# Optimization experiments

Hardware: AMD Instinct MI355X
Metric: run time of the kernel (lower is better)

## Reference

```python
import jax, jax.numpy as jnp
import numpy as np

N, D, E, H, K = 8192, 1024, 8, 256, 2


def setup_inputs() -> dict:
    key = jax.random.key(0)
    ks = jax.random.split(key, 9)
    s = 0.02
    return {
        "x": jax.random.normal(ks[0], (N, D), dtype=jnp.float32),
        "Wg": jax.random.normal(ks[1], (D, E), dtype=jnp.float32) * s,
        "bg": jnp.zeros((E,), dtype=jnp.float32),
        "W1": jax.random.normal(ks[2], (E, D, H), dtype=jnp.float32) * s,
        "b1": jnp.zeros((E, H), dtype=jnp.float32),
        "W2": jax.random.normal(ks[3], (E, H, H), dtype=jnp.float32) * s,
        "b2": jnp.zeros((E, H), dtype=jnp.float32),
        "W3": jax.random.normal(ks[4], (E, H, D), dtype=jnp.float32) * s,
        "b3": jnp.zeros((E, D), dtype=jnp.float32),
    }


def reference(x, Wg, bg, W1, b1, W2, b2, W3, b3):
    # Gating: softmax over experts, then keep only top-k gate values per token.
    gates = jax.nn.softmax(x @ Wg + bg, axis=-1)              # [N, E]
    top_v, top_i = jax.lax.top_k(gates, K)                    # [N, K]
    rows = jnp.arange(gates.shape[0])[:, None]                # [N, 1]
    top_k_gates = jnp.zeros_like(gates).at[rows, top_i].set(top_v)  # [N, E]

    # Dense all-expert MLP (matches original: every expert runs on every token).
    h = jax.nn.relu(jnp.einsum('nd,edh->neh', x, W1) + b1)    # [N, E, H]
    h = jax.nn.relu(jnp.einsum('neh,ehg->neg', h, W2) + b2)   # [N, E, H]  (dropout is eval no-op)
    eo = jax.nn.relu(jnp.einsum('neh,ehd->ned', h, W3) + b3)  # [N, E, D]

    # Combine with masked gates: einsum('...nde,...ne->...nd') with eo in 'ned' layout.
    output = jnp.einsum('ned,ne->nd', eo, top_k_gates)        # [N, D]
    return output
```

## Files before the change

kernel.cpp:

```cpp
#include <hip/hip_runtime.h>
#include <math.h>

#define NTOK 8192
#define DDIM 1024
#define NEXP 8
#define HDIM 256
#define TOPK 2
#define PADM 128
#define CAPS (NTOK * TOPK + NEXP * PADM)
#define NT128 (CAPS / 128)

typedef __attribute__((ext_vector_type(8))) __bf16 bf16x8;
typedef __attribute__((ext_vector_type(4))) float f32x4;

#define GLDS16(g, s)                                                      \
    __builtin_amdgcn_global_load_lds(                                     \
        (const __attribute__((address_space(1))) void*)(g),               \
        (__attribute__((address_space(3))) void*)(s), 16, 0, 0)

static constexpr size_t OFF_TOFF = 128;
static constexpr size_t OFF_ZBUF = 4096;
static constexpr size_t OFF_T2E  = 8192;
static constexpr size_t OFF_T2G  = OFF_T2E + (size_t)NTOK * TOPK * 4;
static constexpr size_t OFF_SLOT = OFF_T2G + (size_t)NTOK * TOPK * 4;
static constexpr size_t OFF_TOK  = OFF_SLOT + (size_t)NTOK * TOPK * 4;
static constexpr size_t OFF_GAT  = OFF_TOK + (size_t)CAPS * 4;
static constexpr size_t OFF_XB   = (OFF_GAT + (size_t)CAPS * 4 + 255) & ~(size_t)255;
static constexpr size_t OFF_W1T  = OFF_XB  + (size_t)NTOK * DDIM * 2;
static constexpr size_t OFF_W2T  = OFF_W1T + (size_t)NEXP * DDIM * HDIM * 2;
static constexpr size_t OFF_W3T  = OFF_W2T + (size_t)NEXP * HDIM * HDIM * 2;
static constexpr size_t OFF_H1   = OFF_W3T + (size_t)NEXP * HDIM * DDIM * 2;
static constexpr size_t OFF_H2   = OFF_H1  + (size_t)CAPS * HDIM * 2;
static constexpr size_t OFF_H3   = OFF_H2  + (size_t)CAPS * HDIM * 2;

static __device__ __forceinline__ unsigned short f2b(float f) {
    __bf16 h = (__bf16)f;
    return __builtin_bit_cast(unsigned short, h);
}
static __device__ __forceinline__ float b2f(unsigned short u) {
    return __builtin_bit_cast(float, ((unsigned)u) << 16);
}

__global__ __launch_bounds__(256) void gate_conv(
    const float* __restrict__ x, const float* __restrict__ Wg,
    const float* __restrict__ bg, unsigned short* __restrict__ xb,
    int* __restrict__ top2e, float* __restrict__ top2g)
{
    const int n = blockIdx.x * 4 + (threadIdx.x >> 6);
    const int lane = threadIdx.x & 63;
    const float* xr = x + (size_t)n * DDIM;
    unsigned short* xbr = xb + (size_t)n * DDIM;

    float acc[NEXP];
#pragma unroll
    for (int e = 0; e < NEXP; ++e) acc[e] = 0.f;

#pragma unroll
    for (int it = 0; it < 4; ++it) {
        const int d = it * 256 + lane * 4;
        const float4 xv = *(const float4*)(xr + d);
        ushort4 u;
        u.x = f2b(xv.x); u.y = f2b(xv.y); u.z = f2b(xv.z); u.w = f2b(xv.w);
        *(ushort4*)(xbr + d) = u;
        const float xa[4] = {xv.x, xv.y, xv.z, xv.w};
#pragma unroll
        for (int q = 0; q < 4; ++q) {
            const float* wr = Wg + (size_t)(d + q) * NEXP;
            const float4 w0 = *(const float4*)wr;
            const float4 w1 = *(const float4*)(wr + 4);
            acc[0] = fmaf(xa[q], w0.x, acc[0]); acc[1] = fmaf(xa[q], w0.y, acc[1]);
            acc[2] = fmaf(xa[q], w0.z, acc[2]); acc[3] = fmaf(xa[q], w0.w, acc[3]);
            acc[4] = fmaf(xa[q], w1.x, acc[4]); acc[5] = fmaf(xa[q], w1.y, acc[5]);
            acc[6] = fmaf(xa[q], w1.z, acc[6]); acc[7] = fmaf(xa[q], w1.w, acc[7]);
        }
    }
#pragma unroll
    for (int off = 32; off > 0; off >>= 1)
#pragma unroll
        for (int e = 0; e < NEXP; ++e) acc[e] += __shfl_down(acc[e], off, 64);

    if (lane == 0) {
        float v[NEXP], mx = -1e30f;
#pragma unroll
        for (int e = 0; e < NEXP; ++e) { v[e] = acc[e] + bg[e]; mx = fmaxf(mx, v[e]); }
        float p[NEXP], s = 0.f;
#pragma unroll
        for (int e = 0; e < NEXP; ++e) { p[e] = expf(v[e] - mx); s += p[e]; }
        const float inv = 1.f / s;
#pragma unroll
        for (int e = 0; e < NEXP; ++e) p[e] *= inv;
        int i0 = 0;
#pragma unroll
        for (int e = 1; e < NEXP; ++e) if (p[e] > p[i0]) i0 = e;
        int i1 = (i0 == 0) ? 1 : 0;
#pragma unroll
        for (int e = 0; e < NEXP; ++e) if (e != i0 && p[e] > p[i1]) i1 = e;
        top2e[n * 2 + 0] = i0;  top2e[n * 2 + 1] = i1;
        top2g[n * 2 + 0] = p[i0]; top2g[n * 2 + 1] = p[i1];
    }
}

__global__ __launch_bounds__(256) void transpose_all(
    const float* __restrict__ W1, const float* __restrict__ W2,
    const float* __restrict__ W3, __bf16* __restrict__ w1t,
    __bf16* __restrict__ w2t, __bf16* __restrict__ w3t)
{
    __shared__ float t[32][33];
    const int e = blockIdx.y;
    int bt = blockIdx.x;
    const float* Wi; __bf16* Wo; int R, C, xt, yt;
    if (bt < 256)      { Wi = W1; Wo = w1t; R = DDIM; C = HDIM; xt = bt & 7;  yt = bt >> 3; }
    else if (bt < 320) { bt -= 256; Wi = W2; Wo = w2t; R = HDIM; C = HDIM; xt = bt & 7;  yt = bt >> 3; }
    else               { bt -= 320; Wi = W3; Wo = w3t; R = HDIM; C = DDIM; xt = bt & 31; yt = bt >> 5; }
    const int r0 = yt * 32, c0 = xt * 32;
    const int tx = threadIdx.x & 31, ty = threadIdx.x >> 5;
    const float* Wie = Wi + (size_t)e * R * C;
    __bf16* Woe = Wo + (size_t)e * C * R;
#pragma unroll
    for (int j = 0; j < 4; ++j)
        t[ty + j * 8][tx] = Wie[(size_t)(r0 + ty + j * 8) * C + c0 + tx];
    __syncthreads();
#pragma unroll
    for (int j = 0; j < 4; ++j)
        Woe[(size_t)(c0 + ty + j * 8) * R + r0 + tx] = (__bf16)t[tx][ty + j * 8];
}

__global__ __launch_bounds__(1024) void route(
    const int* __restrict__ top2e, const float* __restrict__ top2g,
    int* __restrict__ toff, int* __restrict__ tok, float* __restrict__ gat,
    int* __restrict__ slotof, float* __restrict__ zbuf)
{
    const int tid = threadIdx.x;
    const int wv = tid >> 6, ln = tid & 63;
    __shared__ int   waveTot[16][NEXP];
    __shared__ int   waveBase[16][NEXP];
    __shared__ int   totS[NEXP];
    __shared__ int   toffS[NEXP + 1];
    __shared__ short excS[1024][NEXP];

    zbuf[tid] = 0.f;

    int myE[16]; float myG[16];
    const int4*   pe = (const int4*)(top2e + tid * 16);
    const float4* pg = (const float4*)(top2g + tid * 16);
#pragma unroll
    for (int q = 0; q < 4; ++q) {
        const int4 v = pe[q];
        myE[q * 4 + 0] = v.x; myE[q * 4 + 1] = v.y;
        myE[q * 4 + 2] = v.z; myE[q * 4 + 3] = v.w;
        const float4 g = pg[q];
        myG[q * 4 + 0] = g.x; myG[q * 4 + 1] = g.y;
        myG[q * 4 + 2] = g.z; myG[q * 4 + 3] = g.w;
    }

#pragma unroll
    for (int e = 0; e < NEXP; ++e) {
        int c = 0;
#pragma unroll
        for (int j = 0; j < 16; ++j) c += (myE[j] == e);
        int inc = c;
#pragma unroll
        for (int off = 1; off < 64; off <<= 1) {
            const int t = __shfl_up(inc, off, 64);
            if (ln >= off) inc += t;
        }
        excS[tid][e] = (short)(inc - c);
        if (ln == 63) waveTot[wv][e] = inc;
    }
    __syncthreads();

    if (tid < NEXP) {
        int b = 0;
#pragma unroll
        for (int w = 0; w < 16; ++w) {
            const int t = waveTot[w][tid];
            waveBase[w][tid] = b;
            b += t;
        }
        totS[tid] = b;
    }
    __syncthreads();

    if (tid == 0) {
        int acc = 0;
#pragma unroll
        for (int e = 0; e < NEXP; ++e) {
            toffS[e] = acc;
            acc += (totS[e] + PADM - 1) & ~(PADM - 1);
        }
        toffS[NEXP] = acc;
#pragma unroll
        for (int e = 0; e <= NEXP; ++e) toff[e] = toffS[e];
    }
    __syncthreads();

#pragma unroll
    for (int j = 0; j < 16; ++j) {
        int pre = 0;
#pragma unroll
        for (int j2 = 0; j2 < j; ++j2) pre += (myE[j2] == myE[j]);
        const int e = myE[j];
        const int slot = toffS[e] + waveBase[wv][e] + (int)excS[tid][e] + pre;
        const int i = tid * 16 + j;
        tok[slot] = i >> 1;
        gat[slot] = myG[j];
        slotof[i] = slot;
    }

#pragma unroll
    for (int e = 0; e < NEXP; ++e) {
        const int begin = toffS[e] + totS[e];
        const int end   = toffS[e + 1];
        for (int i = begin + tid; i < end; i += 1024) {
            tok[i] = -1;
            gat[i] = 0.f;
        }
    }
}

template<int KDIM, int NCOL, bool GATHER, bool FINAL>
__global__ __launch_bounds__(256) void egemm(
    const __bf16* __restrict__ Ain, const __bf16* __restrict__ Wt,
    const float* __restrict__ ball, const int* __restrict__ toff,
    const int* __restrict__ tok, const float* __restrict__ gat,
    const char* __restrict__ zbuf, __bf16* __restrict__ Out)
{
    const int total = toff[NEXP];
    const int slot0 = blockIdx.x * 128;
    if (slot0 >= total) return;
    int e = 0;
    while (toff[e + 1] <= slot0) ++e;
    const int col0 = blockIdx.y * 128;

    __shared__ __align__(16) char smem[32768];
    char* AsB = smem;
    char* BsB = smem + 16384;

    const int tid  = threadIdx.x;
    const int lane = tid & 63;
    const int wid  = tid >> 6;
    const int wr = wid >> 1, wc = wid & 1;

    const int srow  = tid >> 3;
    const int sslot = tid & 7;
    const __bf16* We = Wt + (size_t)e * NCOL * KDIM;
    const char* ap[4];
    const char* bp[4];
#pragma unroll
    for (int i = 0; i < 4; ++i) {
        const int row = i * 32 + srow;
        const int ks  = sslot ^ (row & 7);
        if (GATHER) {
            const int t = tok[slot0 + row];
            ap[i] = (t >= 0) ? (const char*)(Ain + (size_t)t * KDIM + ks * 8) : zbuf;
        } else {
            ap[i] = (const char*)(Ain + (size_t)(slot0 + row) * KDIM + ks * 8);
        }
        bp[i] = (const char*)(We + (size_t)(col0 + row) * KDIM + ks * 8);
    }

    const int llo = lane & 15, lhi = lane >> 4;
    int abyte[4], am7[4], bbyte[4], bm7[4];
#pragma unroll
    for (int m = 0; m < 4; ++m) {
        const int r = wr * 64 + m * 16 + llo;
        abyte[m] = r * 128; am7[m] = r & 7;
        const int c = wc * 64 + m * 16 + llo;
        bbyte[m] = c * 128; bm7[m] = c & 7;
    }

    f32x4 acc[4][4];
#pragma unroll
    for (int m = 0; m < 4; ++m)
#pragma unroll
        for (int n = 0; n < 4; ++n) acc[m][n] = (f32x4){0.f, 0.f, 0.f, 0.f};

    for (int k0 = 0; k0 < KDIM; k0 += 64) {
        const size_t kb = (size_t)k0 * 2;
#pragma unroll
        for (int i = 0; i < 4; ++i)
            GLDS16(ap[i] + kb, AsB + i * 4096 + wid * 1024);
#pragma unroll
        for (int i = 0; i < 4; ++i)
            GLDS16(bp[i] + kb, BsB + i * 4096 + wid * 1024);
        __syncthreads();
#pragma unroll
        for (int kk = 0; kk < 2; ++kk) {
            bf16x8 af[4], bfr[4];
#pragma unroll
            for (int m = 0; m < 4; ++m)
                af[m] = *(const bf16x8*)(AsB + abyte[m] + ((((kk << 2) + lhi) ^ am7[m]) << 4));
#pragma unroll
            for (int n = 0; n < 4; ++n)
                bfr[n] = *(const bf16x8*)(BsB + bbyte[n] + ((((kk << 2) + lhi) ^ bm7[n]) << 4));
#pragma unroll
            for (int m = 0; m < 4; ++m)
#pragma unroll
                for (int n = 0; n < 4; ++n)
                    acc[m][n] = __builtin_amdgcn_mfma_f32_16x16x32_bf16(
                        af[m], bfr[n], acc[m][n], 0, 0, 0);
        }
        __syncthreads();
    }

    const float* be = ball + (size_t)e * NCOL;
#pragma unroll
    for (int m = 0; m < 4; ++m) {
        const int rbase = slot0 + wr * 64 + m * 16 + lhi * 4;
        float g[4];
        if (FINAL) {
#pragma unroll
            for (int j = 0; j < 4; ++j) g[j] = gat[rbase + j];
        }
#pragma unroll
        for (int n = 0; n < 4; ++n) {
            const int col = col0 + wc * 64 + n * 16 + llo;
            const float bb = be[col];
#pragma unroll
            for (int j = 0; j < 4; ++j) {
                float v = fmaxf(acc[m][n][j] + bb, 0.f);
                if (FINAL) v *= g[j];
                Out[(size_t)(rbase + j) * NCOL + col] = (__bf16)v;
            }
        }
    }
}

__global__ __launch_bounds__(256) void combine(
    const unsigned short* __restrict__ h3, const int* __restrict__ slotof,
    float* __restrict__ out)
{
    const int n = blockIdx.x;
    const int c = threadIdx.x * 4;
    const int s0 = slotof[n * 2], s1 = slotof[n * 2 + 1];
    const ushort4 a = *(const ushort4*)(h3 + (size_t)s0 * DDIM + c);
    const ushort4 b = *(const ushort4*)(h3 + (size_t)s1 * DDIM + c);
    float4 o;
    o.x = b2f(a.x) + b2f(b.x);
    o.y = b2f(a.y) + b2f(b.y);
    o.z = b2f(a.z) + b2f(b.z);
    o.w = b2f(a.w) + b2f(b.w);
    *(float4*)(out + (size_t)n * DDIM + c) = o;
}

extern "C" void kernel_launch(void* const* d_in, const int* in_sizes, int n_in,
                              void* d_out, int out_size, void* d_ws, size_t ws_size,
                              hipStream_t stream)
{
    const float* x  = (const float*)d_in[0];
    const float* Wg = (const float*)d_in[1];
    const float* bg = (const float*)d_in[2];
    const float* W1 = (const float*)d_in[3];
    const float* b1 = (const float*)d_in[4];
    const float* W2 = (const float*)d_in[5];
    const float* b2 = (const float*)d_in[6];
    const float* W3 = (const float*)d_in[7];
    const float* b3 = (const float*)d_in[8];
    float* out = (float*)d_out;

    char* ws = (char*)d_ws;
    int*   toff   = (int*)(ws + OFF_TOFF);
    char*  zbuf   = ws + OFF_ZBUF;
    int*   top2e  = (int*)(ws + OFF_T2E);
    float* top2g  = (float*)(ws + OFF_T2G);
    int*   slotof = (int*)(ws + OFF_SLOT);
    int*   tok    = (int*)(ws + OFF_TOK);
    float* gat    = (float*)(ws + OFF_GAT);
    unsigned short* xbu = (unsigned short*)(ws + OFF_XB);
    __bf16* xb  = (__bf16*)(ws + OFF_XB);
    __bf16* w1t = (__bf16*)(ws + OFF_W1T);
    __bf16* w2t = (__bf16*)(ws + OFF_W2T);
    __bf16* w3t = (__bf16*)(ws + OFF_W3T);
    __bf16* h1  = (__bf16*)(ws + OFF_H1);
    __bf16* h2  = (__bf16*)(ws + OFF_H2);
    __bf16* h3  = (__bf16*)(ws + OFF_H3);

    gate_conv<<<NTOK / 4, 256, 0, stream>>>(x, Wg, bg, xbu, top2e, top2g);
    transpose_all<<<dim3(576, NEXP), 256, 0, stream>>>(W1, W2, W3, w1t, w2t, w3t);
    route<<<1, 1024, 0, stream>>>(top2e, top2g, toff, tok, gat, slotof, (float*)zbuf);

    egemm<DDIM, HDIM, true,  false><<<dim3(NT128, HDIM / 128), 256, 0, stream>>>(
        xb, w1t, b1, toff, tok, gat, zbuf, h1);
    egemm<HDIM, HDIM, false, false><<<dim3(NT128, HDIM / 128), 256, 0, stream>>>(
        h1, w2t, b2, toff, tok, gat, zbuf, h2);
    egemm<HDIM, DDIM, false, true ><<<dim3(NT128, DDIM / 128), 256, 0, stream>>>(
        h2, w3t, b3, toff, tok, gat, zbuf, h3);

    combine<<<NTOK, 256, 0, stream>>>((const unsigned short*)h3, slotof, out);
}
```

Measured before the change: 128.9 us.

## Fuse gating/bf16 conversion and weight transpose into one kernel launch

Merges the gate_conv and transpose_all kernels into a single launch with a 2D grid, where the first 256 x-blocks per y handle gating and the rest transpose weights. Gate weights are now staged in shared memory as expert-major rows, so each lane reads float4 vectors instead of strided global loads. This removes one kernel launch and lets the two independent phases overlap on the GPU. In exchange every block reserves 32KB of shared memory, including the transpose blocks that need far less, which may reduce occupancy.

```diff
diff --git a/kernel.cpp b/kernel.cpp
--- a/kernel.cpp
+++ b/kernel.cpp
@@ -41,88 +41,96 @@
     return __builtin_bit_cast(float, ((unsigned)u) << 16);
 }
 
-__global__ __launch_bounds__(256) void gate_conv(
+__global__ __launch_bounds__(256) void gate_trans(
     const float* __restrict__ x, const float* __restrict__ Wg,
     const float* __restrict__ bg, unsigned short* __restrict__ xb,
-    int* __restrict__ top2e, float* __restrict__ top2g)
-{
-    const int n = blockIdx.x * 4 + (threadIdx.x >> 6);
-    const int lane = threadIdx.x & 63;
-    const float* xr = x + (size_t)n * DDIM;
-    unsigned short* xbr = xb + (size_t)n * DDIM;
-
-    float acc[NEXP];
-#pragma unroll
-    for (int e = 0; e < NEXP; ++e) acc[e] = 0.f;
-
-#pragma unroll
-    for (int it = 0; it < 4; ++it) {
-        const int d = it * 256 + lane * 4;
-        const float4 xv = *(const float4*)(xr + d);
-        ushort4 u;
-        u.x = f2b(xv.x); u.y = f2b(xv.y); u.z = f2b(xv.z); u.w = f2b(xv.w);
-        *(ushort4*)(xbr + d) = u;
-        const float xa[4] = {xv.x, xv.y, xv.z, xv.w};
-#pragma unroll
-        for (int q = 0; q < 4; ++q) {
-            const float* wr = Wg + (size_t)(d + q) * NEXP;
-            const float4 w0 = *(const float4*)wr;
-            const float4 w1 = *(const float4*)(wr + 4);
-            acc[0] = fmaf(xa[q], w0.x, acc[0]); acc[1] = fmaf(xa[q], w0.y, acc[1]);
-            acc[2] = fmaf(xa[q], w0.z, acc[2]); acc[3] = fmaf(xa[q], w0.w, acc[3]);
-            acc[4] = fmaf(xa[q], w1.x, acc[4]); acc[5] = fmaf(xa[q], w1.y, acc[5]);
-            acc[6] = fmaf(xa[q], w1.z, acc[6]); acc[7] = fmaf(xa[q], w1.w, acc[7]);
-        }
-    }
-#pragma unroll
-    for (int off = 32; off > 0; off >>= 1)
-#pragma unroll
-        for (int e = 0; e < NEXP; ++e) acc[e] += __shfl_down(acc[e], off, 64);
-
-    if (lane == 0) {
-        float v[NEXP], mx = -1e30f;
-#pragma unroll
-        for (int e = 0; e < NEXP; ++e) { v[e] = acc[e] + bg[e]; mx = fmaxf(mx, v[e]); }
-        float p[NEXP], s = 0.f;
-#pragma unroll
-        for (int e = 0; e < NEXP; ++e) { p[e] = expf(v[e] - mx); s += p[e]; }
-        const float inv = 1.f / s;
-#pragma unroll
-        for (int e = 0; e < NEXP; ++e) p[e] *= inv;
-        int i0 = 0;
-#pragma unroll
-        for (int e = 1; e < NEXP; ++e) if (p[e] > p[i0]) i0 = e;
-        int i1 = (i0 == 0) ? 1 : 0;
-#pragma unroll
-        for (int e = 0; e < NEXP; ++e) if (e != i0 && p[e] > p[i1]) i1 = e;
-        top2e[n * 2 + 0] = i0;  top2e[n * 2 + 1] = i1;
-        top2g[n * 2 + 0] = p[i0]; top2g[n * 2 + 1] = p[i1];
-    }
-}
-
-__global__ __launch_bounds__(256) void transpose_all(
+    int* __restrict__ top2e, float* __restrict__ top2g,
     const float* __restrict__ W1, const float* __restrict__ W2,
     const float* __restrict__ W3, __bf16* __restrict__ w1t,
     __bf16* __restrict__ w2t, __bf16* __restrict__ w3t)
 {
-    __shared__ float t[32][33];
-    const int e = blockIdx.y;
-    int bt = blockIdx.x;
-    const float* Wi; __bf16* Wo; int R, C, xt, yt;
-    if (bt < 256)      { Wi = W1; Wo = w1t; R = DDIM; C = HDIM; xt = bt & 7;  yt = bt >> 3; }
-    else if (bt < 320) { bt -= 256; Wi = W2; Wo = w2t; R = HDIM; C = HDIM; xt = bt & 7;  yt = bt >> 3; }
-    else               { bt -= 320; Wi = W3; Wo = w3t; R = HDIM; C = DDIM; xt = bt & 31; yt = bt >> 5; }
-    const int r0 = yt * 32, c0 = xt * 32;
-    const int tx = threadIdx.x & 31, ty = threadIdx.x >> 5;
-    const float* Wie = Wi + (size_t)e * R * C;
-    __bf16* Woe = Wo + (size_t)e * C * R;
-#pragma unroll
-    for (int j = 0; j < 4; ++j)
-        t[ty + j * 8][tx] = Wie[(size_t)(r0 + ty + j * 8) * C + c0 + tx];
-    __syncthreads();
-#pragma unroll
-    for (int j = 0; j < 4; ++j)
-        Woe[(size_t)(c0 + ty + j * 8) * R + r0 + tx] = (__bf16)t[tx][ty + j * 8];
+    __shared__ __align__(16) float sh[NEXP * DDIM];
+    const int tid = threadIdx.x;
+
+    if (blockIdx.x < 256) {
+        for (int d = tid; d < DDIM; d += 256) {
+            const float4 w0 = *(const float4*)(Wg + (size_t)d * NEXP);
+            const float4 w1 = *(const float4*)(Wg + (size_t)d * NEXP + 4);
+            sh[0 * DDIM + d] = w0.x; sh[1 * DDIM + d] = w0.y;
+            sh[2 * DDIM + d] = w0.z; sh[3 * DDIM + d] = w0.w;
+            sh[4 * DDIM + d] = w1.x; sh[5 * DDIM + d] = w1.y;
+            sh[6 * DDIM + d] = w1.z; sh[7 * DDIM + d] = w1.w;
+        }
+        __syncthreads();
+
+        const int n = (blockIdx.y * 256 + blockIdx.x) * 4 + (tid >> 6);
+        const int lane = tid & 63;
+        const float* xr = x + (size_t)n * DDIM;
+        unsigned short* xbr = xb + (size_t)n * DDIM;
+
+        float acc[NEXP];
+#pragma unroll
+        for (int e = 0; e < NEXP; ++e) acc[e] = 0.f;
+
+#pragma unroll
+        for (int it = 0; it < 4; ++it) {
+            const int d = it * 256 + lane * 4;
+            const float4 xv = *(const float4*)(xr + d);
+            ushort4 u;
+            u.x = f2b(xv.x); u.y = f2b(xv.y); u.z = f2b(xv.z); u.w = f2b(xv.w);
+            *(ushort4*)(xbr + d) = u;
+#pragma unroll
+            for (int e = 0; e < NEXP; ++e) {
+                const float4 wt = *(const float4*)(sh + e * DDIM + d);
+                acc[e] = fmaf(xv.x, wt.x, acc[e]);
+                acc[e] = fmaf(xv.y, wt.y, acc[e]);
+                acc[e] = fmaf(xv.z, wt.z, acc[e]);
+                acc[e] = fmaf(xv.w, wt.w, acc[e]);
+            }
+        }
+#pragma unroll
+        for (int off = 32; off > 0; off >>= 1)
+#pragma unroll
+            for (int e = 0; e < NEXP; ++e) acc[e] += __shfl_down(acc[e], off, 64);
+
+        if (lane == 0) {
+            float v[NEXP], mx = -1e30f;
+#pragma unroll
+            for (int e = 0; e < NEXP; ++e) { v[e] = acc[e] + bg[e]; mx = fmaxf(mx, v[e]); }
+            float p[NEXP], s = 0.f;
+#pragma unroll
+            for (int e = 0; e < NEXP; ++e) { p[e] = expf(v[e] - mx); s += p[e]; }
+            const float inv = 1.f / s;
+#pragma unroll
+            for (int e = 0; e < NEXP; ++e) p[e] *= inv;
+            int i0 = 0;
+#pragma unroll
+            for (int e = 1; e < NEXP; ++e) if (p[e] > p[i0]) i0 = e;
+            int i1 = (i0 == 0) ? 1 : 0;
+#pragma unroll
+            for (int e = 0; e < NEXP; ++e) if (e != i0 && p[e] > p[i1]) i1 = e;
+            top2e[n * 2 + 0] = i0;  top2e[n * 2 + 1] = i1;
+            top2g[n * 2 + 0] = p[i0]; top2g[n * 2 + 1] = p[i1];
+        }
+    } else {
+        const int e = blockIdx.y;
+        int bt = blockIdx.x - 256;
+        const float* Wi; __bf16* Wo; int R, C, xt, yt;
+        if (bt < 256)      { Wi = W1; Wo = w1t; R = DDIM; C = HDIM; xt = bt & 7;  yt = bt >> 3; }
+        else if (bt < 320) { bt -= 256; Wi = W2; Wo = w2t; R = HDIM; C = HDIM; xt = bt & 7;  yt = bt >> 3; }
+        else               { bt -= 320; Wi = W3; Wo = w3t; R = HDIM; C = DDIM; xt = bt & 31; yt = bt >> 5; }
+        const int r0 = yt * 32, c0 = xt * 32;
+        const int tx = tid & 31, ty = tid >> 5;
+        const float* Wie = Wi + (size_t)e * R * C;
+        __bf16* Woe = Wo + (size_t)e * C * R;
+#pragma unroll
+        for (int j = 0; j < 4; ++j)
+            sh[(ty + j * 8) * 33 + tx] = Wie[(size_t)(r0 + ty + j * 8) * C + c0 + tx];
+        __syncthreads();
+#pragma unroll
+        for (int j = 0; j < 4; ++j)
+            Woe[(size_t)(c0 + ty + j * 8) * R + r0 + tx] = (__bf16)sh[tx * 33 + ty + j * 8];
+    }
 }
 
 __global__ __launch_bounds__(1024) void route(
@@ -375,8 +383,8 @@
     __bf16* h2  = (__bf16*)(ws + OFF_H2);
     __bf16* h3  = (__bf16*)(ws + OFF_H3);
 
-    gate_conv<<<NTOK / 4, 256, 0, stream>>>(x, Wg, bg, xbu, top2e, top2g);
-    transpose_all<<<dim3(576, NEXP), 256, 0, stream>>>(W1, W2, W3, w1t, w2t, w3t);
+    gate_trans<<<dim3(832, NEXP), 256, 0, stream>>>(
+        x, Wg, bg, xbu, top2e, top2g, W1, W2, W3, w1t, w2t, w3t);
     route<<<1, 1024, 0, stream>>>(top2e, top2g, toff, tok, gat, slotof, (float*)zbuf);
 
     egemm<DDIM, HDIM, true,  false><<<dim3(NT128, HDIM / 128), 256, 0, stream>>>(
```

Result: faster. 108.1 us (-16.1%).
